# Kernel optimization log

Measured on AMD Instinct MI355X. Metric: run time of the kernel, lower is better.

## Reference

```python
import jax, jax.numpy as jnp
import numpy as np

B, C, IMG, P, E, H, F, L, NC = 32, 1, 224, 16, 256, 16, 3072, 12, 8
NP_ = (IMG // P) ** 2          # 196 patches
S = NP_ + 1                    # 197 tokens (cls + patches)
HD = E // H                    # 16 head dim
DVL, DVR, DVT = NP_ // 4 + 1, NP_ // 4, NP_ // 4   # 50, 49, 49 -> sum + DVT = 197


def _ln(x, g, b, eps=1e-5):
    m = x.mean(-1, keepdims=True)
    v = ((x - m) ** 2).mean(-1, keepdims=True)
    return (x - m) / jnp.sqrt(v + eps) * g + b


def setup_inputs():
    key = jax.random.key(0)
    ks = iter(jax.random.split(key, 64))
    def w(shape, s=0.02):
        return jax.random.normal(next(ks), shape, jnp.float32) * s
    return dict(
        x=jax.random.normal(next(ks), (B, C, IMG, IMG), jnp.float32),
        W_patch=w((E, C, P, P)), b_patch=jnp.zeros((E,), jnp.float32),
        cls_tok=w((1, 1, E), 1.0), pos_emb=w((1, S, E), 1.0),
        Wkl=w((E, E)), bkl=jnp.zeros((E,), jnp.float32),
        Wvl=w((DVL, E)), bvl=jnp.zeros((DVL,), jnp.float32),
        Wkr=w((E, E)), bkr=jnp.zeros((E,), jnp.float32),
        Wvr=w((DVR, E)), bvr=jnp.zeros((DVR,), jnp.float32),
        Wkt=w((E, E)), bkt=jnp.zeros((E,), jnp.float32),
        Wvt=w((DVT, E)), bvt=jnp.zeros((DVT,), jnp.float32),
        ln1_g=jnp.ones((L, E), jnp.float32), ln1_b=jnp.zeros((L, E), jnp.float32),
        Wqkv=w((L, 3 * E, E)), bqkv=jnp.zeros((L, 3 * E), jnp.float32),
        Wo=w((L, E, E)), bo=jnp.zeros((L, E), jnp.float32),
        ln2_g=jnp.ones((L, E), jnp.float32), ln2_b=jnp.zeros((L, E), jnp.float32),
        W1=w((L, F, E)), b1=jnp.zeros((L, F), jnp.float32),
        W2=w((L, E, F)), b2=jnp.zeros((L, E), jnp.float32),
        lnf_g=jnp.ones((E,), jnp.float32), lnf_b=jnp.zeros((E,), jnp.float32),
        W_head=w((NC, E)), b_head=jnp.zeros((NC,), jnp.float32),
    )


def reference(x, W_patch, b_patch, cls_tok, pos_emb,
              Wkl, bkl, Wvl, bvl, Wkr, bkr, Wvr, bvr, Wkt, bkt, Wvt, bvt,
              ln1_g, ln1_b, Wqkv, bqkv, Wo, bo, ln2_g, ln2_b, W1, b1, W2, b2,
              lnf_g, lnf_b, W_head, b_head):
    Bsz = x.shape[0]
    scale_k = 1.0 / jnp.sqrt(jnp.float32(E))
    # patch embedding: conv with stride == kernel == patch size
    h = jax.lax.conv_general_dilated(x, W_patch, (P, P), 'VALID',
                                     dimension_numbers=('NCHW', 'OIHW', 'NCHW'))
    h = h + b_patch[None, :, None, None]                   # (B, E, 14, 14)
    h = h.reshape(Bsz, E, NP_).transpose(0, 2, 1)          # (B, 196, E)
    h = jnp.concatenate([jnp.broadcast_to(cls_tok, (Bsz, 1, E)), h], 1) + pos_emb

    # linear rotatory attention fusing each sample with its batch neighbors
    def rag(xl, xt, xr):                                   # each (S, E)
        rt = xt.mean(0)                                    # target summary (E,)
        al = jax.nn.softmax((xl @ Wkl.T + bkl) @ rt * scale_k)
        rl = al @ (xl @ Wvl.T + bvl)                       # (DVL,)
        ar = jax.nn.softmax((xr @ Wkr.T + bkr) @ rt * scale_k)
        rr = ar @ (xr @ Wvr.T + bvr)                       # (DVR,)
        kt = xt @ Wkt.T + bkt
        vt = xt @ Wvt.T + bvt
        rtl = jax.nn.softmax(kt @ xl.mean(0) * scale_k) @ vt   # (DVT,)
        rtr = jax.nn.softmax(kt @ xr.mean(0) * scale_k) @ vt   # (DVT,)
        f = jnp.concatenate([rl, rtl, rtr, rr])            # (S,) = 50+49+49+49
        return jnp.outer(f, rt)                            # (S, E)

    mid = jax.vmap(rag)(h[:-2], h[1:-1], h[2:])            # (B-2, S, E) batched (no per-sample loop)
    h = jnp.concatenate([h[:1], mid, h[-1:]], 0)

    # standard pre-LN transformer encoder, scanned over stacked layer params
    def block(carry, p):
        g1, b1n, wqkv, bq, wo, bo_, g2, b2n, w1, bb1, w2, bb2 = p
        xn = _ln(carry, g1, b1n)
        qkv = xn @ wqkv.T + bq                             # (B, S, 3E)
        q, k, v = jnp.split(qkv, 3, axis=-1)
        q = q.reshape(Bsz, S, H, HD)
        k = k.reshape(Bsz, S, H, HD)
        v = v.reshape(Bsz, S, H, HD)
        att = jnp.einsum('bqhd,bkhd->bhqk', q, k) / jnp.sqrt(jnp.float32(HD))
        att = jax.nn.softmax(att, axis=-1)
        o = jnp.einsum('bhqk,bkhd->bqhd', att, v).reshape(Bsz, S, E)
        carry = carry + o @ wo.T + bo_
        xn2 = _ln(carry, g2, b2n)
        ff = jax.nn.gelu(xn2 @ w1.T + bb1, approximate=False) @ w2.T + bb2
        return carry + ff, None

    h, _ = jax.lax.scan(block, h, (ln1_g, ln1_b, Wqkv, bqkv, Wo, bo,
                                   ln2_g, ln2_b, W1, b1, W2, b2))
    cls = _ln(h[:, 0], lnf_g, lnf_b)
    return cls @ W_head.T + b_head
```

## Files before the change

kernel.cpp:

```cpp
#include <hip/hip_runtime.h>
#include <hip/hip_bf16.h>
#include <math.h>

constexpr int Bz  = 32;
constexpr int S   = 197;
constexpr int E   = 256;
constexpr int Hn  = 16;
constexpr int HD  = 16;
constexpr int Fd  = 3072;
constexpr int Ln  = 12;
constexpr int MS  = Bz * S;
constexpr int MP  = 6400;
constexpr int NPAT = 6272;
constexpr int DVL = 50, DVR = 49, DVT = 49;
constexpr size_t WLSTRIDE = 1835008;

typedef __attribute__((ext_vector_type(8))) short short8;
typedef __attribute__((ext_vector_type(4))) short short4v;
typedef __attribute__((ext_vector_type(4))) float f32x4;

__device__ __forceinline__ unsigned short f2bf(float f) {
    unsigned int u = __float_as_uint(f);
    u = (u + 0x7FFFu + ((u >> 16) & 1u)) >> 16;
    return (unsigned short)u;
}

__device__ __forceinline__ void gload_lds16(const void* g, void* l) {
    __builtin_amdgcn_global_load_lds(
        (const __attribute__((address_space(1))) void*)g,
        (__attribute__((address_space(3))) void*)l, 16, 0, 0);
}

__device__ __forceinline__ float wave_reduce(float v, int op) {
    #pragma unroll
    for (int off = 32; off > 0; off >>= 1) {
        float o = __shfl_xor(v, off, 64);
        v = op ? fmaxf(v, o) : v + o;
    }
    return v;
}

__device__ __forceinline__ float block_reduce(float v, float* red4, int op) {
    v = wave_reduce(v, op);
    int w = threadIdx.x >> 6;
    if ((threadIdx.x & 63) == 0) red4[w] = v;
    __syncthreads();
    float r = op ? fmaxf(fmaxf(red4[0], red4[1]), fmaxf(red4[2], red4[3]))
                 : (red4[0] + red4[1] + red4[2] + red4[3]);
    __syncthreads();
    return r;
}

__device__ __forceinline__ float gelu_f(float v) {
    float v2 = v * v;
    float e  = __expf(v * fmaf(-0.071354816f, v2, -1.5957691f));
    return __fdividef(v, 1.0f + e);
}

__global__ __launch_bounds__(256) void patchify_kernel(
        const float* __restrict__ x, unsigned short* __restrict__ Ab) {
    int pi = blockIdx.x;
    int b = pi / 196, q = pi % 196;
    int i = q / 14, j = q % 14;
    int e = threadIdx.x, pr = e >> 4, pc = e & 15;
    float v = x[((size_t)(b * 224 + i * 16 + pr)) * 224 + j * 16 + pc];
    Ab[(size_t)pi * 256 + e] = f2bf(v);
}

__global__ __launch_bounds__(256) void cls_pos_kernel(
        const float* __restrict__ cls, const float* __restrict__ pos,
        float* __restrict__ h0) {
    int b = blockIdx.x, e = threadIdx.x;
    h0[(size_t)(b * S) * E + e] = cls[e] + pos[e];
}

__global__ __launch_bounds__(256) void convert_kernel(
        const float* __restrict__ src, unsigned short* __restrict__ dst) {
    int i4 = (blockIdx.x * 256 + threadIdx.x) * 4;
    float4 v = *(const float4*)(src + i4);
    ushort4 o;
    o.x = f2bf(v.x); o.y = f2bf(v.y); o.z = f2bf(v.z); o.w = f2bf(v.w);
    *(ushort4*)(dst + i4) = o;
}

__global__ __launch_bounds__(256) void convert_w_all_kernel(
        const float* __restrict__ wqkv, const float* __restrict__ wo,
        const float* __restrict__ w1, const float* __restrict__ w2,
        unsigned short* __restrict__ out) {
    size_t idx = (size_t)blockIdx.x * 256 + threadIdx.x;
    int l = (int)(idx / 458752);
    int r4 = (int)(idx % 458752) * 4;
    const float* src;
    if (r4 < 196608)       src = wqkv + (size_t)l * 196608 + r4;
    else if (r4 < 262144)  src = wo   + (size_t)l * 65536  + (r4 - 196608);
    else if (r4 < 1048576) src = w1   + (size_t)l * 786432 + (r4 - 262144);
    else                   src = w2   + (size_t)l * 786432 + (r4 - 1048576);
    float4 v = *(const float4*)src;
    ushort4 o;
    o.x = f2bf(v.x); o.y = f2bf(v.y); o.z = f2bf(v.z); o.w = f2bf(v.w);
    *(ushort4*)(out + (size_t)l * WLSTRIDE + r4) = o;
}

__global__ __launch_bounds__(256) void means_kernel(
        const float* __restrict__ h0, float* __restrict__ M) {
    __shared__ float part[4][256];
    int b = blockIdx.x, tid = threadIdx.x, w = tid >> 6, lane = tid & 63;
    float4 a = {0.f, 0.f, 0.f, 0.f};
    for (int t = w; t < S; t += 4) {
        float4 v = *(const float4*)&h0[((size_t)(b * S + t)) * E + lane * 4];
        a.x += v.x; a.y += v.y; a.z += v.z; a.w += v.w;
    }
    *(float4*)&part[w][lane * 4] = a;
    __syncthreads();
    M[b * E + tid] = (part[0][tid] + part[1][tid] + part[2][tid] + part[3][tid])
                     * (1.f / (float)S);
}

__global__ __launch_bounds__(256) void uvec_kernel(
        const float* __restrict__ M,
        const float* __restrict__ Wkl, const float* __restrict__ bkl,
        const float* __restrict__ Wkr, const float* __restrict__ bkr,
        const float* __restrict__ Wkt, const float* __restrict__ bkt,
        float* __restrict__ Ul, float* __restrict__ Ur, float* __restrict__ Ut,
        float* __restrict__ cl, float* __restrict__ cr, float* __restrict__ ct) {
    __shared__ float p0[4][256], p1[4][256], p2[4][256], red4[4];
    int t = blockIdx.x, tid = threadIdx.x, w = tid >> 6, lane = tid & 63;
    const float* mt = M + t * E;
    float4 a0 = {0,0,0,0}, a1 = {0,0,0,0}, a2 = {0,0,0,0};
    for (int i = w * 64; i < w * 64 + 64; i++) {
        float mi = mt[i];
        float4 v0 = *(const float4*)&Wkl[(size_t)i * 256 + lane * 4];
        float4 v1 = *(const float4*)&Wkr[(size_t)i * 256 + lane * 4];
        float4 v2 = *(const float4*)&Wkt[(size_t)i * 256 + lane * 4];
        a0.x += v0.x * mi; a0.y += v0.y * mi; a0.z += v0.z * mi; a0.w += v0.w * mi;
        a1.x += v1.x * mi; a1.y += v1.y * mi; a1.z += v1.z * mi; a1.w += v1.w * mi;
        a2.x += v2.x * mi; a2.y += v2.y * mi; a2.z += v2.z * mi; a2.w += v2.w * mi;
    }
    *(float4*)&p0[w][lane * 4] = a0;
    *(float4*)&p1[w][lane * 4] = a1;
    *(float4*)&p2[w][lane * 4] = a2;
    __syncthreads();
    Ul[t * E + tid] = p0[0][tid] + p0[1][tid] + p0[2][tid] + p0[3][tid];
    Ur[t * E + tid] = p1[0][tid] + p1[1][tid] + p1[2][tid] + p1[3][tid];
    Ut[t * E + tid] = p2[0][tid] + p2[1][tid] + p2[2][tid] + p2[3][tid];
    float me = mt[tid];
    float c0 = block_reduce(bkl[tid] * me, red4, 0);
    float c1 = block_reduce(bkr[tid] * me, red4, 0);
    float c2 = block_reduce(bkt[tid] * me, red4, 0);
    if (tid == 0) { cl[t] = c0; cr[t] = c1; ct[t] = c2; }
}

__global__ __launch_bounds__(256) void rag_score_kernel(
        const float* __restrict__ h0, const float* __restrict__ M,
        const float* __restrict__ Ul, const float* __restrict__ Ur,
        const float* __restrict__ Ut,
        const float* __restrict__ cl, const float* __restrict__ cr,
        const float* __restrict__ ct,
        const float* __restrict__ Wvl, const float* __restrict__ bvl,
        const float* __restrict__ Wvr, const float* __restrict__ bvr,
        const float* __restrict__ Wvt, const float* __restrict__ bvt,
        float* __restrict__ fbuf) {
    int t = blockIdx.x >> 2, br = blockIdx.x & 3;
    const float* xsrc; const float* u; float c;
    const float* Wv; const float* bv; int dv, fo;
    if (br == 0)      { xsrc = h0 + (size_t)t * S * E;       u = Ul + (t+1)*E; c = cl[t+1]; Wv = Wvl; bv = bvl; dv = DVL; fo = 0; }
    else if (br == 1) { xsrc = h0 + (size_t)(t+1) * S * E;   u = Ut + t*E;     c = ct[t];   Wv = Wvt; bv = bvt; dv = DVT; fo = DVL; }
    else if (br == 2) { xsrc = h0 + (size_t)(t+1) * S * E;   u = Ut + (t+2)*E; c = ct[t+2]; Wv = Wvt; bv = bvt; dv = DVT; fo = DVL + DVT; }
    else              { xsrc = h0 + (size_t)(t+2) * S * E;   u = Ur + (t+1)*E; c = cr[t+1]; Wv = Wvr; bv = bvr; dv = DVR; fo = DVL + 2*DVT; }
    __shared__ float us[256], sc[200], xbar[256], part[4][256], red4[4];
    int tid = threadIdx.x, w = tid >> 6, lane = tid & 63;
    us[tid] = u[tid];
    __syncthreads();
    float4 u4 = *(float4*)&us[lane * 4];
    for (int s = w; s < S; s += 4) {
        float4 x4 = *(const float4*)&xsrc[(size_t)s * E + lane * 4];
        float p = x4.x*u4.x + x4.y*u4.y + x4.z*u4.z + x4.w*u4.w;
        p = wave_reduce(p, 0);
        if (lane == 0) sc[s] = (p + c) * 0.0625f;
    }
    __syncthreads();
    float v = (tid < S) ? sc[tid] : -1e30f;
    float mx = block_reduce(v, red4, 1);
    float ex = (tid < S) ? expf(v - mx) : 0.f;
    float dn = block_reduce(ex, red4, 0);
    if (tid < S) sc[tid] = ex / dn;
    __syncthreads();
    float4 pa = {0.f, 0.f, 0.f, 0.f};
    for (int s = w; s < S; s += 4) {
        float a = sc[s];
        float4 x4 = *(const float4*)&xsrc[(size_t)s * E + lane * 4];
        pa.x += a * x4.x; pa.y += a * x4.y; pa.z += a * x4.z; pa.w += a * x4.w;
    }
    *(float4*)&part[w][lane * 4] = pa;
    __syncthreads();
    xbar[tid] = part[0][tid] + part[1][tid] + part[2][tid] + part[3][tid];
    __syncthreads();
    float4 xb4 = *(float4*)&xbar[lane * 4];
    for (int d = w; d < dv; d += 4) {
        float4 w4 = *(const float4*)&Wv[(size_t)d * E + lane * 4];
        float p = w4.x*xb4.x + w4.y*xb4.y + w4.z*xb4.z + w4.w*xb4.w;
        p = wave_reduce(p, 0);
        if (lane == 0) fbuf[t * 256 + fo + d] = p + bv[d];
    }
}

__global__ __launch_bounds__(256) void rag_outer_kernel(
        const float* __restrict__ fbuf, const float* __restrict__ M,
        float* __restrict__ h1) {
    int bid = blockIdx.x;
    int t = bid / S, s = bid % S;
    float f = fbuf[t * 256 + s];
    int e = threadIdx.x;
    h1[((size_t)((t + 1) * S + s)) * E + e] = f * M[(t + 1) * E + e];
}

__global__ __launch_bounds__(256) void copy_edges(const float* __restrict__ h0,
                                                  float* __restrict__ h1) {
    int i = blockIdx.x * 256 + threadIdx.x;
    int n = S * E;
    if (i < n) h1[i] = h0[i];
    else if (i < 2 * n) {
        int j = i - n;
        size_t o = (size_t)31 * S * E + j;
        h1[o] = h0[o];
    }
}

__global__ __launch_bounds__(256) void ln_kernel(const float* __restrict__ in,
                                                 unsigned short* __restrict__ out,
                                                 const float* __restrict__ g,
                                                 const float* __restrict__ b) {
    int w = threadIdx.x >> 6, lane = threadIdx.x & 63;
    int tok = blockIdx.x * 4 + w;
    const float* row = in + (size_t)tok * E;
    float4 v = *(const float4*)&row[lane * 4];
    float mean = wave_reduce(v.x + v.y + v.z + v.w, 0) * (1.f / 256.f);
    float dx = v.x - mean, dy = v.y - mean, dz = v.z - mean, dw = v.w - mean;
    float var = wave_reduce(dx*dx + dy*dy + dz*dz + dw*dw, 0) * (1.f / 256.f);
    float inv = rsqrtf(var + 1e-5f);
    float4 gg = *(const float4*)&g[lane * 4];
    float4 bb = *(const float4*)&b[lane * 4];
    ushort4 o;
    o.x = f2bf(dx * inv * gg.x + bb.x);
    o.y = f2bf(dy * inv * gg.y + bb.y);
    o.z = f2bf(dz * inv * gg.z + bb.z);
    o.w = f2bf(dw * inv * gg.w + bb.w);
    *(ushort4*)&out[(size_t)tok * E + lane * 4] = o;
}

template <int MODE>
__global__ __launch_bounds__(256) void gemm_s64(
        const unsigned short* __restrict__ A, int lda,
        const unsigned short* __restrict__ W, int ldw,
        const float* __restrict__ bias,
        void* __restrict__ Cv, int ldc, int K, int MT, int NT,
        const float* __restrict__ pos) {
    constexpr bool SWAP = (MODE == 4);
    __shared__ unsigned short As[2 * 64 * 64];
    __shared__ unsigned short Bs[2 * 64 * 64];
    const int id = blockIdx.x;
    const int mt = (id & 7) + 8 * (id / (8 * NT));
    const int nt = (id >> 3) % NT;
    if (mt >= MT) return;
    if (MODE == 5) {
        A += (size_t)blockIdx.y * K;
        W += (size_t)blockIdx.y * K;
    }
    const int m0 = mt * 64, n0 = nt * 64;
    const int tid = threadIdx.x, wave = tid >> 6, lane = tid & 63;
    const int lr = lane & 15, kg = lane >> 4;
    const int srow = wave * 16 + (lane >> 3);
    const int scol = ((lane & 7) ^ (lane >> 3)) * 8;
    auto stage = [&](int bb, int k0) {
        #pragma unroll
        for (int q = 0; q < 2; q++) {
            gload_lds16(&A[(size_t)(m0 + srow + q * 8) * lda + k0 + scol],
                        &As[bb * 4096 + (wave * 16 + q * 8) * 64]);
            gload_lds16(&W[(size_t)(n0 + srow + q * 8) * ldw + k0 + scol],
                        &Bs[bb * 4096 + (wave * 16 + q * 8) * 64]);
        }
    };
    const int nIter = K >> 6;
    stage(0, 0);
    f32x4 acc[4] = {};
    for (int i = 0; i < nIter; i++) {
        __syncthreads();
        if (i + 1 < nIter) stage((i + 1) & 1, (i + 1) * 64);
        const int bb = i & 1;
        #pragma unroll
        for (int h = 0; h < 2; h++) {
            const int sw = ((h * 4 + kg) ^ (lr & 7)) * 8;
            short8 af = *(short8*)&As[bb * 4096 + (wave * 16 + lr) * 64 + sw];
            #pragma unroll
            for (int j = 0; j < 4; j++) {
                short8 bf = *(short8*)&Bs[bb * 4096 + (j * 16 + lr) * 64 + sw];
                if (SWAP)
                    acc[j] = __builtin_amdgcn_mfma_f32_16x16x32_bf16(bf, af, acc[j], 0, 0, 0);
                else
                    acc[j] = __builtin_amdgcn_mfma_f32_16x16x32_bf16(af, bf, acc[j], 0, 0, 0);
            }
        }
    }
    if (SWAP) {
        __syncthreads();
        unsigned short* T = As + wave * 1152;
        #pragma unroll
        for (int j = 0; j < 4; j++) {
            int nb = n0 + j * 16 + kg * 4;
            float4 b4 = *(const float4*)&bias[nb];
            ushort4 pk;
            pk.x = f2bf(acc[j][0] + b4.x);
            pk.y = f2bf(acc[j][1] + b4.y);
            pk.z = f2bf(acc[j][2] + b4.z);
            pk.w = f2bf(acc[j][3] + b4.w);
            *(ushort4*)&T[lr * 72 + j * 16 + kg * 4] = pk;
        }
        int rrow = lane >> 3, cg = (lane & 7) * 8;
        #pragma unroll
        for (int g = 0; g < 2; g++) {
            int row = g * 8 + rrow;
            short8 val = *(short8*)&T[row * 72 + cg];
            int m = m0 + wave * 16 + row;
            *(short8*)&((unsigned short*)Cv)[(size_t)m * ldc + n0 + cg] = val;
        }
    } else {
        #pragma unroll
        for (int j = 0; j < 4; j++) {
            int n = n0 + j * 16 + lr;
            float bv = (bias && (MODE != 5 || blockIdx.y == 0)) ? bias[n] : 0.f;
            #pragma unroll
            for (int r = 0; r < 4; r++) {
                int m = m0 + wave * 16 + kg * 4 + r;
                float v = acc[j][r] + bv;
                if (MODE == 1) ((float*)Cv)[(size_t)m * ldc + n] += v;
                if (MODE == 5) atomicAdd(&((float*)Cv)[(size_t)m * ldc + n], v);
                if (MODE == 3) {
                    int b = m / 196, s = m - b * 196 + 1;
                    ((float*)Cv)[((size_t)(b * S + s)) * E + n] = v + pos[(size_t)s * E + n];
                }
            }
        }
    }
}

template <int JC, int MODE, bool GELU>
__global__ __launch_bounds__(256, 4) void gemm_k256(
        const unsigned short* __restrict__ A,
        const unsigned short* __restrict__ W,
        const float* __restrict__ bias,
        void* __restrict__ Cv, int ldc, int MT, int NT) {
    constexpr int LDA = 256, LDW = 256;
    constexpr int BN = 64 * JC;
    __shared__ unsigned short As[4 * 64 * 64];
    const int id = blockIdx.x;
    const int mt = (id & 7) + 8 * (id / (8 * NT));
    const int nt = (id >> 3) % NT;
    if (mt >= MT) return;
    const int m0 = mt * 64, n0 = nt * BN;
    const int tid = threadIdx.x, wave = tid >> 6, lane = tid & 63;
    const int lr = lane & 15, kg = lane >> 4;
    const int wn = wave * (JC * 16);
    const int srow = wave * 16 + (lane >> 3);
    const int scol = ((lane & 7) ^ (lane >> 3)) * 8;
    #pragma unroll
    for (int c = 0; c < 4; c++)
        #pragma unroll
        for (int q = 0; q < 2; q++)
            gload_lds16(&A[(size_t)(m0 + srow + q * 8) * LDA + c * 64 + scol],
                        &As[c * 4096 + (wave * 16 + q * 8) * 64]);
    const unsigned short* Wrow[JC];
    #pragma unroll
    for (int j = 0; j < JC; j++)
        Wrow[j] = W + (size_t)(n0 + wn + j * 16 + lr) * LDW + kg * 8;
    f32x4 acc[4][JC] = {};
    short8 bufA[JC], bufB[JC];
    auto loadB = [&](short8 (&dst)[JC], int s) {
        #pragma unroll
        for (int j = 0; j < JC; j++)
            dst[j] = *(const short8*)(Wrow[j] + s * 32);
    };
    loadB(bufA, 0);
    __syncthreads();
    #pragma unroll
    for (int s = 0; s < 8; s++) {
        const int c = s >> 1, h = s & 1;
        const int sw = ((h * 4 + kg) ^ (lr & 7)) * 8;
        short8 (&cur)[JC] = (s & 1) ? bufB : bufA;
        short8 (&nxt)[JC] = (s & 1) ? bufA : bufB;
        if (s < 7) loadB(nxt, s + 1);
        #pragma unroll
        for (int i2 = 0; i2 < 4; i2++) {
            short8 af = *(short8*)&As[c * 4096 + (i2 * 16 + lr) * 64 + sw];
            #pragma unroll
            for (int j = 0; j < JC; j++)
                acc[i2][j] = __builtin_amdgcn_mfma_f32_16x16x32_bf16(
                        cur[j], af, acc[i2][j], 0, 0, 0);
        }
    }
    if (MODE == 1) {
        #pragma unroll
        for (int i2 = 0; i2 < 4; i2++)
            #pragma unroll
            for (int j = 0; j < JC; j++) {
                int m = m0 + i2 * 16 + lr;
                int n = n0 + wn + j * 16 + kg * 4;
                float* dst = (float*)Cv + (size_t)m * ldc + n;
                float4 o4 = *(float4*)dst;
                float4 b4 = *(const float4*)&bias[n];
                o4.x += acc[i2][j][0] + b4.x;
                o4.y += acc[i2][j][1] + b4.y;
                o4.z += acc[i2][j][2] + b4.z;
                o4.w += acc[i2][j][3] + b4.w;
                *(float4*)dst = o4;
            }
        return;
    }
    __syncthreads();
    constexpr int TS = JC * 16 + 4;
    unsigned short* T = As + wave * (64 * TS);
    #pragma unroll
    for (int i2 = 0; i2 < 4; i2++)
        #pragma unroll
        for (int j = 0; j < JC; j++) {
            int nb = n0 + wn + j * 16 + kg * 4;
            float4 b4 = *(const float4*)&bias[nb];
            float vx = acc[i2][j][0] + b4.x;
            float vy = acc[i2][j][1] + b4.y;
            float vz = acc[i2][j][2] + b4.z;
            float vw = acc[i2][j][3] + b4.w;
            if (GELU) { vx = gelu_f(vx); vy = gelu_f(vy);
                        vz = gelu_f(vz); vw = gelu_f(vw); }
            ushort4 pk;
            pk.x = f2bf(vx); pk.y = f2bf(vy); pk.z = f2bf(vz); pk.w = f2bf(vw);
            *(ushort4*)&T[(i2 * 16 + lr) * TS + j * 16 + kg * 4] = pk;
        }
    if (JC == 2) {
        int rr = lane >> 2, cc = (lane & 3) * 8;
        #pragma unroll
        for (int g = 0; g < 4; g++) {
            int row = g * 16 + rr;
            short8 val = *(short8*)&T[row * TS + cc];
            *(short8*)&((unsigned short*)Cv)[(size_t)(m0 + row) * ldc + n0 + wn + cc] = val;
        }
    } else {
        int rr = lane >> 1, cc = (lane & 1) * 8;
        #pragma unroll
        for (int g = 0; g < 2; g++) {
            int row = g * 32 + rr;
            short8 val = *(short8*)&T[row * TS + cc];
            *(short8*)&((unsigned short*)Cv)[(size_t)(m0 + row) * ldc + n0 + wn + cc] = val;
        }
    }
}

static inline int sg(int MT, int NT) { return ((MT + 7) / 8) * 8 * NT; }

__global__ __launch_bounds__(256) void attn_kernel(
        const unsigned short* __restrict__ qkv, unsigned short* __restrict__ o) {
    int b = blockIdx.x >> 4, hh = blockIdx.x & 15;
    __shared__ unsigned short Qs[208][32];
    __shared__ unsigned short Ks[208][32];
    __shared__ unsigned short Vt[16][224];
    __shared__ unsigned short Ps[4][16][224];
    int tid = threadIdx.x, wave = tid >> 6, lane = tid & 63;
    int lr = lane & 15, kg = lane >> 4;
    short8 z8 = {};
    if (tid < 208) {
        if (tid < 197) {
            size_t row = (size_t)(b * S + tid) * 768 + hh * 16;
            *(short8*)&Qs[tid][0] = *(const short8*)&qkv[row];
            *(short8*)&Qs[tid][8] = *(const short8*)&qkv[row + 8];
            *(short8*)&Ks[tid][0] = *(const short8*)&qkv[row + 256];
            *(short8*)&Ks[tid][8] = *(const short8*)&qkv[row + 264];
            union { short8 v8[2]; unsigned short u[16]; } vv;
            vv.v8[0] = *(const short8*)&qkv[row + 512];
            vv.v8[1] = *(const short8*)&qkv[row + 520];
            #pragma unroll
            for (int d = 0; d < 16; d++) Vt[d][tid] = vv.u[d];
        } else {
            *(short8*)&Qs[tid][0] = z8; *(short8*)&Qs[tid][8] = z8;
            *(short8*)&Ks[tid][0] = z8; *(short8*)&Ks[tid][8] = z8;
            #pragma unroll
            for (int d = 0; d < 16; d++) Vt[d][tid] = 0;
        }
        *(short8*)&Qs[tid][16] = z8; *(short8*)&Qs[tid][24] = z8;
        *(short8*)&Ks[tid][16] = z8; *(short8*)&Ks[tid][24] = z8;
    } else if (tid < 224) {
        #pragma unroll
        for (int d = 0; d < 16; d++) Vt[d][tid] = 0;
    }
    {
        short4v z4 = {};
        *(short4v*)&Ps[wave][lane >> 2][208 + (lane & 3) * 4] = z4;
    }
    __syncthreads();
    const f32x4 zf = {0.f, 0.f, 0.f, 0.f};
    for (int it = wave; it < 13; it += 4) {
        short8 qa = *(short8*)&Qs[it * 16 + lr][kg * 8];
        f32x4 sc[13];
        #pragma unroll
        for (int j = 0; j < 13; j++) {
            short8 kb = *(short8*)&Ks[j * 16 + lr][kg * 8];
            sc[j] = __builtin_amdgcn_mfma_f32_16x16x32_bf16(qa, kb, zf, 0, 0, 0);
        }
        float m[4] = {-1e30f, -1e30f, -1e30f, -1e30f};
        #pragma unroll
        for (int j = 0; j < 13; j++) {
            if (j * 16 + lr < 197) {
                #pragma unroll
                for (int r = 0; r < 4; r++) m[r] = fmaxf(m[r], sc[j][r]);
            }
        }
        #pragma unroll
        for (int off = 1; off < 16; off <<= 1)
            #pragma unroll
            for (int r = 0; r < 4; r++) m[r] = fmaxf(m[r], __shfl_xor(m[r], off, 64));
        float l[4] = {0.f, 0.f, 0.f, 0.f};
        #pragma unroll
        for (int j = 0; j < 13; j++) {
            bool valid = (j * 16 + lr) < 197;
            #pragma unroll
            for (int r = 0; r < 4; r++) {
                float p = valid ? __expf((sc[j][r] - m[r]) * 0.25f) : 0.f;
                l[r] += p;
                Ps[wave][kg * 4 + r][j * 16 + lr] = f2bf(p);
            }
        }
        #pragma unroll
        for (int off = 1; off < 16; off <<= 1)
            #pragma unroll
            for (int r = 0; r < 4; r++) l[r] += __shfl_xor(l[r], off, 64);
        f32x4 oa = zf;
        #pragma unroll
        for (int k0 = 0; k0 < 224; k0 += 32) {
            short8 pa = *(short8*)&Ps[wave][lr][k0 + kg * 8];
            short8 vb = *(short8*)&Vt[lr][k0 + kg * 8];
            oa = __builtin_amdgcn_mfma_f32_16x16x32_bf16(pa, vb, oa, 0, 0, 0);
        }
        #pragma unroll
        for (int r = 0; r < 4; r++) {
            int q = it * 16 + kg * 4 + r;
            if (q < 197)
                o[((size_t)(b * S + q)) * 256 + hh * 16 + lr] = f2bf(oa[r] / l[r]);
        }
    }
}

__global__ __launch_bounds__(256) void head_kernel(
        const float* __restrict__ h, const float* __restrict__ g,
        const float* __restrict__ bb, const float* __restrict__ Wh,
        const float* __restrict__ bh, float* __restrict__ out) {
    __shared__ float red4[4];
    __shared__ float xs[256];
    int b = blockIdx.x, e = threadIdx.x;
    float v = h[((size_t)(b * S)) * E + e];
    float mean = block_reduce(v, red4, 0) * (1.f / 256.f);
    float d = v - mean;
    float var = block_reduce(d * d, red4, 0) * (1.f / 256.f);
    float xn = d * rsqrtf(var + 1e-5f) * g[e] + bb[e];
    xs[e] = xn;
    __syncthreads();
    for (int n = 0; n < 8; n++) {
        float s = block_reduce(xs[e] * Wh[(size_t)n * 256 + e], red4, 0);
        if (e == 0) out[b * 8 + n] = s + bh[n];
    }
}

extern "C" void kernel_launch(void* const* d_in, const int* in_sizes, int n_in,
                              void* d_out, int out_size, void* d_ws, size_t ws_size,
                              hipStream_t stream) {
    const float* x      = (const float*)d_in[0];
    const float* W_patch= (const float*)d_in[1];
    const float* b_patch= (const float*)d_in[2];
    const float* cls_tok= (const float*)d_in[3];
    const float* pos_emb= (const float*)d_in[4];
    const float* Wkl = (const float*)d_in[5];   const float* bkl = (const float*)d_in[6];
    const float* Wvl = (const float*)d_in[7];   const float* bvl = (const float*)d_in[8];
    const float* Wkr = (const float*)d_in[9];   const float* bkr = (const float*)d_in[10];
    const float* Wvr = (const float*)d_in[11];  const float* bvr = (const float*)d_in[12];
    const float* Wkt = (const float*)d_in[13];  const float* bkt = (const float*)d_in[14];
    const float* Wvt = (const float*)d_in[15];  const float* bvt = (const float*)d_in[16];
    const float* ln1_g = (const float*)d_in[17]; const float* ln1_b = (const float*)d_in[18];
    const float* Wqkv  = (const float*)d_in[19]; const float* bqkv  = (const float*)d_in[20];
    const float* Wo    = (const float*)d_in[21]; const float* bo    = (const float*)d_in[22];
    const float* ln2_g = (const float*)d_in[23]; const float* ln2_b = (const float*)d_in[24];
    const float* W1 = (const float*)d_in[25];   const float* b1 = (const float*)d_in[26];
    const float* W2 = (const float*)d_in[27];   const float* b2 = (const float*)d_in[28];
    const float* lnf_g = (const float*)d_in[29]; const float* lnf_b = (const float*)d_in[30];
    const float* W_head = (const float*)d_in[31]; const float* b_head = (const float*)d_in[32];

    char* p = (char*)d_ws;
    float* h0 = (float*)p;                    p += (size_t)MP * 256 * 4;
    float* h1 = (float*)p;                    p += (size_t)MP * 256 * 4;
    unsigned short* qkb = (unsigned short*)p; p += (size_t)MP * 768 * 2;
    unsigned short* xnb = (unsigned short*)p; p += (size_t)MP * 256 * 2;
    unsigned short* ob  = (unsigned short*)p; p += (size_t)MP * 256 * 2;
    unsigned short* ff  = (unsigned short*)p; p += (size_t)MP * 3072 * 2;
    unsigned short* wpb = (unsigned short*)p; p += (size_t)65536 * 2;
    float* ragws = (float*)p;                 p += (size_t)40960 * 4;
    unsigned short* wall = (unsigned short*)p;
    float* M    = ragws;
    float* Ul   = ragws + 8192;
    float* Ur   = ragws + 2 * 8192;
    float* Ut   = ragws + 3 * 8192;
    float* cl   = ragws + 4 * 8192;
    float* cr   = cl + 32;
    float* ct   = cl + 64;
    float* fbuf = cl + 96;

    convert_w_all_kernel<<<21504, 256, 0, stream>>>(Wqkv, Wo, W1, W2, wall);

    convert_kernel<<<64, 256, 0, stream>>>(W_patch, wpb);
    patchify_kernel<<<NPAT, 256, 0, stream>>>(x, xnb);
    cls_pos_kernel<<<Bz, 256, 0, stream>>>(cls_tok, pos_emb, h0);
    gemm_s64<3><<<sg(98, 4), 256, 0, stream>>>(
        xnb, 256, wpb, 256, b_patch, h0, 256, 256, 98, 4, pos_emb);

    means_kernel<<<Bz, 256, 0, stream>>>(h0, M);
    uvec_kernel<<<Bz, 256, 0, stream>>>(M, Wkl, bkl, Wkr, bkr, Wkt, bkt,
                                        Ul, Ur, Ut, cl, cr, ct);
    rag_score_kernel<<<(Bz - 2) * 4, 256, 0, stream>>>(
        h0, M, Ul, Ur, Ut, cl, cr, ct, Wvl, bvl, Wvr, bvr, Wvt, bvt, fbuf);
    rag_outer_kernel<<<(Bz - 2) * S, 256, 0, stream>>>(fbuf, M, h1);
    copy_edges<<<(2 * S * E + 255) / 256, 256, 0, stream>>>(h0, h1);

    for (int l = 0; l < Ln; l++) {
        const unsigned short* wqkv_b = wall + (size_t)l * WLSTRIDE;
        const unsigned short* wo_b   = wqkv_b + 196608;
        const unsigned short* w1_b   = wqkv_b + 262144;
        const unsigned short* w2_b   = wqkv_b + 1048576;
        ln_kernel<<<MS / 4, 256, 0, stream>>>(h1, xnb, ln1_g + l * E, ln1_b + l * E);
        gemm_k256<1, 4, false><<<sg(100, 12), 256, 0, stream>>>(
            xnb, wqkv_b, bqkv + l * 768, qkb, 768, 100, 12);
        attn_kernel<<<Bz * Hn, 256, 0, stream>>>(qkb, ob);
        gemm_k256<1, 1, false><<<sg(100, 4), 256, 0, stream>>>(
            ob, wo_b, bo + l * 256, h1, 256, 100, 4);
        ln_kernel<<<MS / 4, 256, 0, stream>>>(h1, xnb, ln2_g + l * E, ln2_b + l * E);
        gemm_k256<2, 4, true><<<sg(100, 24), 256, 0, stream>>>(
            xnb, w1_b, b1 + l * Fd, ff, 3072, 100, 24);
        gemm_s64<5><<<dim3(sg(100, 4), 4), 256, 0, stream>>>(
            ff, 3072, w2_b, 3072, b2 + l * 256, h1, 256, 768, 100, 4, nullptr);
    }
    head_kernel<<<Bz, 256, 0, stream>>>(h1, lnf_g, lnf_b, W_head, b_head, (float*)d_out);
}
```

Measured before the change: 1.642 ms.

## Add split-K FFN2 GEMM kernel and widen parallelism in RAG prologue kernels

Replaces the FFN down-projection GEMM (previously split-K by 4 with K=768 chunks) with a dedicated kernel that splits K into 12 chunks of 256. It stages the whole A chunk in LDS at once, streams W fragments from global memory into registers, and reduces the partial results with atomics. The goal is more blocks in flight and less LDS pipelining overhead, at the cost of three times as many atomicAdds on the fp32 residual. The RAG prologue also changes: uvec is split across a 2D grid of matrix and column chunks, and rag_score now runs with 512 threads using a custom wave-level softmax reduction. Unused MODE 4/5 paths are removed from gemm_s64.

Result: slower. 4.085 ms (+148.8%).

```diff
diff --git a/kernel.cpp b/kernel.cpp
--- a/kernel.cpp
+++ b/kernel.cpp
@@ -123,34 +123,30 @@
         const float* __restrict__ Wkt, const float* __restrict__ bkt,
         float* __restrict__ Ul, float* __restrict__ Ur, float* __restrict__ Ut,
         float* __restrict__ cl, float* __restrict__ cr, float* __restrict__ ct) {
-    __shared__ float p0[4][256], p1[4][256], p2[4][256], red4[4];
-    int t = blockIdx.x, tid = threadIdx.x, w = tid >> 6, lane = tid & 63;
+    __shared__ float part[4][64], red4[4];
+    int t = blockIdx.x, yy = blockIdx.y;
+    int mat = yy >> 2, ec = yy & 3, e0 = ec * 64;
+    const float* Wk = (mat == 0) ? Wkl : (mat == 1) ? Wkr : Wkt;
+    const float* bk = (mat == 0) ? bkl : (mat == 1) ? bkr : bkt;
+    float* U  = (mat == 0) ? Ul  : (mat == 1) ? Ur  : Ut;
+    float* co = (mat == 0) ? cl  : (mat == 1) ? cr  : ct;
+    int tid = threadIdx.x, ig = tid >> 6, col = tid & 63;
     const float* mt = M + t * E;
-    float4 a0 = {0,0,0,0}, a1 = {0,0,0,0}, a2 = {0,0,0,0};
-    for (int i = w * 64; i < w * 64 + 64; i++) {
-        float mi = mt[i];
-        float4 v0 = *(const float4*)&Wkl[(size_t)i * 256 + lane * 4];
-        float4 v1 = *(const float4*)&Wkr[(size_t)i * 256 + lane * 4];
-        float4 v2 = *(const float4*)&Wkt[(size_t)i * 256 + lane * 4];
-        a0.x += v0.x * mi; a0.y += v0.y * mi; a0.z += v0.z * mi; a0.w += v0.w * mi;
-        a1.x += v1.x * mi; a1.y += v1.y * mi; a1.z += v1.z * mi; a1.w += v1.w * mi;
-        a2.x += v2.x * mi; a2.y += v2.y * mi; a2.z += v2.z * mi; a2.w += v2.w * mi;
-    }
-    *(float4*)&p0[w][lane * 4] = a0;
-    *(float4*)&p1[w][lane * 4] = a1;
-    *(float4*)&p2[w][lane * 4] = a2;
-    __syncthreads();
-    Ul[t * E + tid] = p0[0][tid] + p0[1][tid] + p0[2][tid] + p0[3][tid];
-    Ur[t * E + tid] = p1[0][tid] + p1[1][tid] + p1[2][tid] + p1[3][tid];
-    Ut[t * E + tid] = p2[0][tid] + p2[1][tid] + p2[2][tid] + p2[3][tid];
-    float me = mt[tid];
-    float c0 = block_reduce(bkl[tid] * me, red4, 0);
-    float c1 = block_reduce(bkr[tid] * me, red4, 0);
-    float c2 = block_reduce(bkt[tid] * me, red4, 0);
-    if (tid == 0) { cl[t] = c0; cr[t] = c1; ct[t] = c2; }
-}
-
-__global__ __launch_bounds__(256) void rag_score_kernel(
+    float a = 0.f;
+    #pragma unroll 4
+    for (int i = ig * 64; i < ig * 64 + 64; i++)
+        a += Wk[(size_t)i * 256 + e0 + col] * mt[i];
+    part[ig][col] = a;
+    __syncthreads();
+    if (tid < 64)
+        U[t * E + e0 + tid] = part[0][tid] + part[1][tid] + part[2][tid] + part[3][tid];
+    if (ec == 0) {
+        float c = block_reduce(bk[tid] * mt[tid], red4, 0);
+        if (tid == 0) co[t] = c;
+    }
+}
+
+__global__ __launch_bounds__(512) void rag_score_kernel(
         const float* __restrict__ h0, const float* __restrict__ M,
         const float* __restrict__ Ul, const float* __restrict__ Ur,
         const float* __restrict__ Ut,
@@ -167,12 +163,12 @@
     else if (br == 1) { xsrc = h0 + (size_t)(t+1) * S * E;   u = Ut + t*E;     c = ct[t];   Wv = Wvt; bv = bvt; dv = DVT; fo = DVL; }
     else if (br == 2) { xsrc = h0 + (size_t)(t+1) * S * E;   u = Ut + (t+2)*E; c = ct[t+2]; Wv = Wvt; bv = bvt; dv = DVT; fo = DVL + DVT; }
     else              { xsrc = h0 + (size_t)(t+2) * S * E;   u = Ur + (t+1)*E; c = cr[t+1]; Wv = Wvr; bv = bvr; dv = DVR; fo = DVL + 2*DVT; }
-    __shared__ float us[256], sc[200], xbar[256], part[4][256], red4[4];
+    __shared__ float us[256], sc[200], xbar[256], part[8][256], red8[8];
     int tid = threadIdx.x, w = tid >> 6, lane = tid & 63;
-    us[tid] = u[tid];
+    if (tid < 256) us[tid] = u[tid];
     __syncthreads();
     float4 u4 = *(float4*)&us[lane * 4];
-    for (int s = w; s < S; s += 4) {
+    for (int s = w; s < S; s += 8) {
         float4 x4 = *(const float4*)&xsrc[(size_t)s * E + lane * 4];
         float p = x4.x*u4.x + x4.y*u4.y + x4.z*u4.z + x4.w*u4.w;
         p = wave_reduce(p, 0);
@@ -180,23 +176,37 @@
     }
     __syncthreads();
     float v = (tid < S) ? sc[tid] : -1e30f;
-    float mx = block_reduce(v, red4, 1);
-    float ex = (tid < S) ? expf(v - mx) : 0.f;
-    float dn = block_reduce(ex, red4, 0);
+    float vr = wave_reduce(v, 1);
+    if (lane == 0) red8[w] = vr;
+    __syncthreads();
+    float mx = red8[0];
+    #pragma unroll
+    for (int i = 1; i < 8; i++) mx = fmaxf(mx, red8[i]);
+    float ex = (tid < S) ? __expf(v - mx) : 0.f;
+    float er = wave_reduce(ex, 0);
+    __syncthreads();
+    if (lane == 0) red8[w] = er;
+    __syncthreads();
+    float dn = red8[0] + red8[1] + red8[2] + red8[3]
+             + red8[4] + red8[5] + red8[6] + red8[7];
     if (tid < S) sc[tid] = ex / dn;
     __syncthreads();
     float4 pa = {0.f, 0.f, 0.f, 0.f};
-    for (int s = w; s < S; s += 4) {
+    for (int s = w; s < S; s += 8) {
         float a = sc[s];
         float4 x4 = *(const float4*)&xsrc[(size_t)s * E + lane * 4];
         pa.x += a * x4.x; pa.y += a * x4.y; pa.z += a * x4.z; pa.w += a * x4.w;
     }
     *(float4*)&part[w][lane * 4] = pa;
     __syncthreads();
-    xbar[tid] = part[0][tid] + part[1][tid] + part[2][tid] + part[3][tid];
+    if (tid < 256) {
+        float xb = part[0][tid] + part[1][tid] + part[2][tid] + part[3][tid]
+                 + part[4][tid] + part[5][tid] + part[6][tid] + part[7][tid];
+        xbar[tid] = xb;
+    }
     __syncthreads();
     float4 xb4 = *(float4*)&xbar[lane * 4];
-    for (int d = w; d < dv; d += 4) {
+    for (int d = w; d < dv; d += 8) {
         float4 w4 = *(const float4*)&Wv[(size_t)d * E + lane * 4];
         float p = w4.x*xb4.x + w4.y*xb4.y + w4.z*xb4.z + w4.w*xb4.w;
         p = wave_reduce(p, 0);
@@ -255,17 +265,12 @@
         const float* __restrict__ bias,
         void* __restrict__ Cv, int ldc, int K, int MT, int NT,
         const float* __restrict__ pos) {
-    constexpr bool SWAP = (MODE == 4);
     __shared__ unsigned short As[2 * 64 * 64];
     __shared__ unsigned short Bs[2 * 64 * 64];
     const int id = blockIdx.x;
     const int mt = (id & 7) + 8 * (id / (8 * NT));
     const int nt = (id >> 3) % NT;
     if (mt >= MT) return;
-    if (MODE == 5) {
-        A += (size_t)blockIdx.y * K;
-        W += (size_t)blockIdx.y * K;
-    }
     const int m0 = mt * 64, n0 = nt * 64;
     const int tid = threadIdx.x, wave = tid >> 6, lane = tid & 63;
     const int lr = lane & 15, kg = lane >> 4;
@@ -294,50 +299,22 @@
             #pragma unroll
             for (int j = 0; j < 4; j++) {
                 short8 bf = *(short8*)&Bs[bb * 4096 + (j * 16 + lr) * 64 + sw];
-                if (SWAP)
-                    acc[j] = __builtin_amdgcn_mfma_f32_16x16x32_bf16(bf, af, acc[j], 0, 0, 0);
-                else
-                    acc[j] = __builtin_amdgcn_mfma_f32_16x16x32_bf16(af, bf, acc[j], 0, 0, 0);
+                acc[j] = __builtin_amdgcn_mfma_f32_16x16x32_bf16(af, bf, acc[j], 0, 0, 0);
             }
         }
     }
-    if (SWAP) {
-        __syncthreads();
-        unsigned short* T = As + wave * 1152;
-        #pragma unroll
-        for (int j = 0; j < 4; j++) {
-            int nb = n0 + j * 16 + kg * 4;
-            float4 b4 = *(const float4*)&bias[nb];
-            ushort4 pk;
-            pk.x = f2bf(acc[j][0] + b4.x);
-            pk.y = f2bf(acc[j][1] + b4.y);
-            pk.z = f2bf(acc[j][2] + b4.z);
-            pk.w = f2bf(acc[j][3] + b4.w);
-            *(ushort4*)&T[lr * 72 + j * 16 + kg * 4] = pk;
-        }
-        int rrow = lane >> 3, cg = (lane & 7) * 8;
-        #pragma unroll
-        for (int g = 0; g < 2; g++) {
-            int row = g * 8 + rrow;
-            short8 val = *(short8*)&T[row * 72 + cg];
-            int m = m0 + wave * 16 + row;
-            *(short8*)&((unsigned short*)Cv)[(size_t)m * ldc + n0 + cg] = val;
-        }
-    } else {
-        #pragma unroll
-        for (int j = 0; j < 4; j++) {
-            int n = n0 + j * 16 + lr;
-            float bv = (bias && (MODE != 5 || blockIdx.y == 0)) ? bias[n] : 0.f;
-            #pragma unroll
-            for (int r = 0; r < 4; r++) {
-                int m = m0 + wave * 16 + kg * 4 + r;
-                float v = acc[j][r] + bv;
-                if (MODE == 1) ((float*)Cv)[(size_t)m * ldc + n] += v;
-                if (MODE == 5) atomicAdd(&((float*)Cv)[(size_t)m * ldc + n], v);
-                if (MODE == 3) {
-                    int b = m / 196, s = m - b * 196 + 1;
-                    ((float*)Cv)[((size_t)(b * S + s)) * E + n] = v + pos[(size_t)s * E + n];
-                }
+    #pragma unroll
+    for (int j = 0; j < 4; j++) {
+        int n = n0 + j * 16 + lr;
+        float bv = bias ? bias[n] : 0.f;
+        #pragma unroll
+        for (int r = 0; r < 4; r++) {
+            int m = m0 + wave * 16 + kg * 4 + r;
+            float v = acc[j][r] + bv;
+            if (MODE == 1) ((float*)Cv)[(size_t)m * ldc + n] += v;
+            if (MODE == 3) {
+                int b = m / 196, s = m - b * 196 + 1;
+                ((float*)Cv)[((size_t)(b * S + s)) * E + n] = v + pos[(size_t)s * E + n];
             }
         }
     }
@@ -449,6 +426,63 @@
             int row = g * 32 + rr;
             short8 val = *(short8*)&T[row * TS + cc];
             *(short8*)&((unsigned short*)Cv)[(size_t)(m0 + row) * ldc + n0 + wn + cc] = val;
+        }
+    }
+}
+
+__global__ __launch_bounds__(256, 4) void gemm_ffn2(
+        const unsigned short* __restrict__ A,
+        const unsigned short* __restrict__ W,
+        const float* __restrict__ bias,
+        float* __restrict__ C,
+        int MT, int NT) {
+    constexpr int LDA = 3072, LDW = 3072;
+    __shared__ unsigned short As[4 * 64 * 64];
+    const int id = blockIdx.x;
+    const int mt = (id & 7) + 8 * (id / (8 * NT));
+    const int nt = (id >> 3) % NT;
+    if (mt >= MT) return;
+    const int kofs = blockIdx.y * 256;
+    const int m0 = mt * 64, n0 = nt * 64;
+    const int tid = threadIdx.x, wave = tid >> 6, lane = tid & 63;
+    const int lr = lane & 15, kg = lane >> 4;
+    const int wn = wave * 16;
+    const int srow = wave * 16 + (lane >> 3);
+    const int scol = ((lane & 7) ^ (lane >> 3)) * 8;
+    #pragma unroll
+    for (int c = 0; c < 4; c++)
+        #pragma unroll
+        for (int q = 0; q < 2; q++)
+            gload_lds16(&A[(size_t)(m0 + srow + q * 8) * LDA + kofs + c * 64 + scol],
+                        &As[c * 4096 + (wave * 16 + q * 8) * 64]);
+    const unsigned short* Wrow = W + (size_t)(n0 + wn + lr) * LDW + kofs + kg * 8;
+    f32x4 acc[4] = {};
+    short8 bufA, bufB;
+    bufA = *(const short8*)(Wrow);
+    __syncthreads();
+    #pragma unroll
+    for (int s = 0; s < 8; s++) {
+        const int c = s >> 1, h = s & 1;
+        const int sw = ((h * 4 + kg) ^ (lr & 7)) * 8;
+        short8 cur = (s & 1) ? bufB : bufA;
+        if (s < 7) { if (s & 1) bufA = *(const short8*)(Wrow + (s + 1) * 32);
+                     else       bufB = *(const short8*)(Wrow + (s + 1) * 32); }
+        #pragma unroll
+        for (int i2 = 0; i2 < 4; i2++) {
+            short8 af = *(short8*)&As[c * 4096 + (i2 * 16 + lr) * 64 + sw];
+            acc[i2] = __builtin_amdgcn_mfma_f32_16x16x32_bf16(cur, af, acc[i2], 0, 0, 0);
+        }
+    }
+    const bool addb = (blockIdx.y == 0);
+    #pragma unroll
+    for (int i2 = 0; i2 < 4; i2++) {
+        int m = m0 + i2 * 16 + lr;
+        int n = n0 + wn + kg * 4;
+        float* dst = C + (size_t)m * 256 + n;
+        #pragma unroll
+        for (int r = 0; r < 4; r++) {
+            float v = acc[i2][r] + (addb ? bias[n + r] : 0.f);
+            atomicAdd(dst + r, v);
         }
     }
 }
@@ -617,9 +651,9 @@
         xnb, 256, wpb, 256, b_patch, h0, 256, 256, 98, 4, pos_emb);
 
     means_kernel<<<Bz, 256, 0, stream>>>(h0, M);
-    uvec_kernel<<<Bz, 256, 0, stream>>>(M, Wkl, bkl, Wkr, bkr, Wkt, bkt,
-                                        Ul, Ur, Ut, cl, cr, ct);
-    rag_score_kernel<<<(Bz - 2) * 4, 256, 0, stream>>>(
+    uvec_kernel<<<dim3(Bz, 12), 256, 0, stream>>>(M, Wkl, bkl, Wkr, bkr, Wkt, bkt,
+                                                  Ul, Ur, Ut, cl, cr, ct);
+    rag_score_kernel<<<(Bz - 2) * 4, 512, 0, stream>>>(
         h0, M, Ul, Ur, Ut, cl, cr, ct, Wvl, bvl, Wvr, bvr, Wvt, bvt, fbuf);
     rag_outer_kernel<<<(Bz - 2) * S, 256, 0, stream>>>(fbuf, M, h1);
     copy_edges<<<(2 * S * E + 255) / 256, 256, 0, stream>>>(h0, h1);
@@ -638,8 +672,8 @@
         ln_kernel<<<MS / 4, 256, 0, stream>>>(h1, xnb, ln2_g + l * E, ln2_b + l * E);
         gemm_k256<2, 4, true><<<sg(100, 24), 256, 0, stream>>>(
             xnb, w1_b, b1 + l * Fd, ff, 3072, 100, 24);
-        gemm_s64<5><<<dim3(sg(100, 4), 4), 256, 0, stream>>>(
-            ff, 3072, w2_b, 3072, b2 + l * 256, h1, 256, 768, 100, 4, nullptr);
+        gemm_ffn2<<<dim3(sg(100, 4), 12), 256, 0, stream>>>(
+            ff, w2_b, b2 + l * 256, h1, 100, 4);
     }
     head_kernel<<<Bz, 256, 0, stream>>>(h1, lnf_g, lnf_b, W_head, b_head, (float*)d_out);
 }
```
